# Optimization experiments

Hardware: AMD Instinct MI355X
Metric: run time of the kernel (lower is better)

## Reference

```python
import jax, jax.numpy as jnp
import numpy as np

EMBED_DIM = 1024
NUM_HEADS = 16
HEAD_DIM = EMBED_DIM // NUM_HEADS
B, S = 2, 2048


def setup_inputs() -> dict:
    key = jax.random.key(0)
    ks = jax.random.split(key, 9)
    d = EMBED_DIM
    scale = 1.0 / np.sqrt(d)
    inp = {
        "x": jax.random.normal(ks[0], (B, S, d), dtype=jnp.float32),
        "mask": jnp.ones((B, S), dtype=jnp.int32),
        "Wq": jax.random.normal(ks[1], (d, d), dtype=jnp.float32) * scale,
        "bq": jnp.zeros((d,), dtype=jnp.float32),
        "Wk": jax.random.normal(ks[2], (d, d), dtype=jnp.float32) * scale,
        "bk": jnp.zeros((d,), dtype=jnp.float32),
        "Wv": jax.random.normal(ks[3], (d, d), dtype=jnp.float32) * scale,
        "bv": jnp.zeros((d,), dtype=jnp.float32),
        "Wo": jax.random.normal(ks[4], (d, d), dtype=jnp.float32) * scale,
        "bo": jnp.zeros((d,), dtype=jnp.float32),
    }
    return inp


def reference(x, mask, Wq, bq, Wk, bk, Wv, bv, Wo, bo):
    b, s, _ = x.shape
    # projections; torch Linear computes x @ W.T + b
    q = (x @ Wq.T + bq).reshape(b, s, NUM_HEADS, HEAD_DIM).transpose(0, 2, 1, 3)
    k = (x @ Wk.T + bk).reshape(b, s, NUM_HEADS, HEAD_DIM).transpose(0, 2, 1, 3)
    v = (x @ Wv.T + bv).reshape(b, s, NUM_HEADS, HEAD_DIM).transpose(0, 2, 1, 3)
    scores = jnp.einsum("bhqd,bhkd->bhqk", q, k) / np.sqrt(HEAD_DIM)  # (B,H,S,S)
    m = (mask == 0)[:, None, None, :]  # broadcast over heads and query pos
    scores = jnp.where(m, jnp.float32(-1e9), scores)
    attn = jax.nn.softmax(scores, axis=-1)
    out = jnp.einsum("bhqk,bhkd->bhqd", attn, v)
    out = out.transpose(0, 2, 1, 3).reshape(b, s, EMBED_DIM)
    return out @ Wo.T + bo
```

## Files before the change

kernel.cpp:

```cpp
#include <hip/hip_runtime.h>

#define EMBED 1024
#define NHEAD 16
#define HDIM  64
#define BB    2
#define SS    2048

typedef __bf16 bf16x8 __attribute__((ext_vector_type(8)));
typedef float  f32x4  __attribute__((ext_vector_type(4)));
typedef _Float16 f16x4 __attribute__((ext_vector_type(4)));
typedef __fp16 hf16x2 __attribute__((ext_vector_type(2)));

#if defined(__has_builtin)
#if __has_builtin(__builtin_amdgcn_exp2f)
#define EXP2(x) __builtin_amdgcn_exp2f(x)
#else
#define EXP2(x) exp2f(x)
#endif
#else
#define EXP2(x) exp2f(x)
#endif

__device__ __forceinline__ unsigned short f2bf(float f) {
  union { float f; unsigned u; } v; v.f = f;
  unsigned r = v.u + 0x7fffu + ((v.u >> 16) & 1u);
  return (unsigned short)(r >> 16);
}

__device__ __forceinline__ float bf2f(unsigned short u) {
  union { unsigned u; float f; } v; v.u = ((unsigned)u) << 16;
  return v.f;
}

__device__ __forceinline__ unsigned short f2h(float f) {
  union { _Float16 h; unsigned short u; } t;
  t.h = (_Float16)f;
  return t.u;
}

__device__ __forceinline__ void g2l16(const unsigned short* g, unsigned short* l) {
  __builtin_amdgcn_global_load_lds(
      (const __attribute__((address_space(1))) unsigned int*)g,
      (__attribute__((address_space(3))) unsigned int*)l, 16, 0, 0);
}

__global__ __launch_bounds__(256)
void cvt5_kernel(const float* __restrict__ x,  const float* __restrict__ Wq,
                 const float* __restrict__ Wk, const float* __restrict__ Wv,
                 const float* __restrict__ Wo, const int* __restrict__ mask,
                 unsigned short* __restrict__ xb,  unsigned short* __restrict__ Wqb,
                 unsigned short* __restrict__ Wkb, unsigned short* __restrict__ Wvb,
                 unsigned short* __restrict__ Wob, float* __restrict__ mbias) {
  const int i = blockIdx.x * 256 + threadIdx.x;
  if (i < (1 << 21)) {
    const float* src;
    unsigned short* dst;
    int j;
    if (i < (1 << 20)) {
      src = x; dst = xb; j = i;
    } else {
      const int t = i - (1 << 20);
      const int r = t >> 18;
      j = t & ((1 << 18) - 1);
      src = (r == 0) ? Wq : (r == 1) ? Wk : (r == 2) ? Wv : Wo;
      dst = (r == 0) ? Wqb : (r == 1) ? Wkb : (r == 2) ? Wvb : Wob;
    }
    const float4 f = ((const float4*)src)[j];
    ushort4 u;
    u.x = f2bf(f.x); u.y = f2bf(f.y); u.z = f2bf(f.z); u.w = f2bf(f.w);
    ((ushort4*)dst)[j] = u;
  } else {
    const int j = i - (1 << 21);
    const int4 m = ((const int4*)mask)[j];
    float4 o;
    o.x = m.x ? 0.f : -1e30f; o.y = m.y ? 0.f : -1e30f;
    o.z = m.z ? 0.f : -1e30f; o.w = m.w ? 0.f : -1e30f;
    ((float4*)mbias)[j] = o;
  }
}

template <typename EpiFn>
__device__ __forceinline__
void gemm_core(const unsigned short* __restrict__ A,
               const unsigned short* __restrict__ Bm,
               int m0, int n0, EpiFn epi) {
  __shared__ unsigned short sA[128 * 64];
  __shared__ unsigned short sB[128 * 64];
  const int tid = threadIdx.x;
  const int l  = tid & 63;
  const int w  = tid >> 6;
  const int lm = l & 15;
  const int qd = l >> 4;
  const int wm = w & 1;
  const int wn = w >> 1;

  f32x4 acc[4][4];
#pragma unroll
  for (int i = 0; i < 4; ++i)
#pragma unroll
    for (int j = 0; j < 4; ++j) acc[i][j] = (f32x4){0.f, 0.f, 0.f, 0.f};

  for (int k0 = 0; k0 < EMBED; k0 += 64) {
#pragma unroll
    for (int i = 0; i < 4; ++i) {
      const int t = i * 256 + tid;
      const int r = t >> 3;
      const int c = (t & 7) ^ (r & 7);
      g2l16(A + (m0 + r) * EMBED + k0 + c * 8, &sA[(i * 256 + (w << 6)) * 8]);
      g2l16(Bm + (n0 + r) * EMBED + k0 + c * 8, &sB[(i * 256 + (w << 6)) * 8]);
    }
    __syncthreads();
#pragma unroll
    for (int kk = 0; kk < 2; ++kk) {
      bf16x8 af[4], bfr[4];
#pragma unroll
      for (int mi = 0; mi < 4; ++mi) {
        const int R = wm * 64 + mi * 16 + lm;
        const int ch = R * 8 + (((kk << 2) + qd) ^ (R & 7));
        af[mi] = *(const bf16x8*)&sA[ch * 8];
      }
#pragma unroll
      for (int ni = 0; ni < 4; ++ni) {
        const int R = wn * 64 + ni * 16 + lm;
        const int ch = R * 8 + (((kk << 2) + qd) ^ (R & 7));
        bfr[ni] = *(const bf16x8*)&sB[ch * 8];
      }
#pragma unroll
      for (int mi = 0; mi < 4; ++mi)
#pragma unroll
        for (int ni = 0; ni < 4; ++ni)
          acc[mi][ni] = __builtin_amdgcn_mfma_f32_16x16x32_bf16(
              af[mi], bfr[ni], acc[mi][ni], 0, 0, 0);
    }
    __syncthreads();
  }

#pragma unroll
  for (int mi = 0; mi < 4; ++mi)
#pragma unroll
    for (int ni = 0; ni < 4; ++ni) {
      const int mb = m0 + wm * 64 + mi * 16 + qd * 4;
      const int n  = n0 + wn * 64 + ni * 16 + lm;
      epi(acc[mi][ni], mb, n);
    }
}

__device__ __forceinline__ void decode_tile(int flat, int& a0, int& b0) {
  const int sub = flat & 15;
  const int g = flat >> 4;
  a0 = ((g >> 2) * 2 + (sub >> 3));
  b0 = ((g & 3) * 8 + (sub & 7));
}

__global__ __launch_bounds__(256)
void gemm_qkv(const unsigned short* __restrict__ xb,
              const unsigned short* __restrict__ Wqb,
              const unsigned short* __restrict__ Wkb,
              const unsigned short* __restrict__ Wvb,
              const float* __restrict__ bq, const float* __restrict__ bk,
              const float* __restrict__ bv,
              unsigned short* __restrict__ Qb, unsigned short* __restrict__ Kb,
              unsigned short* __restrict__ VTb) {
  const int z = blockIdx.y;
  int a0, b0;
  decode_tile(blockIdx.x, a0, b0);
  if (z < 2) {
    const unsigned short* A = z ? Wkb : Wqb;
    const float* bias = z ? bk : bq;
    unsigned short* O = z ? Kb : Qb;
    const float scale = z ? 1.0f : 0.125f * 1.4426950408889634f;
    gemm_core(A, xb, a0 * 128, b0 * 128, [&](const f32x4& v, int mb, int n) {
      const float4 bvv = *(const float4*)&bias[mb];
      const int h = mb >> 6, d0 = mb & 63;
      const int b = n >> 11, s = n & 2047;
      ushort4 u;
      u.x = f2bf((v.x + bvv.x) * scale); u.y = f2bf((v.y + bvv.y) * scale);
      u.z = f2bf((v.z + bvv.z) * scale); u.w = f2bf((v.w + bvv.w) * scale);
      *(ushort4*)&O[(((b * NHEAD + h) * SS) + s) * HDIM + d0] = u;
    });
  } else {
    gemm_core(xb, Wvb, b0 * 128, a0 * 128, [&](const f32x4& v, int mb, int n) {
      const float bvv = bv[n];
      const int b = mb >> 11, s = mb & 2047;
      const int h = n >> 6, d = n & 63;
      ushort4 u;
      u.x = f2h(v.x + bvv); u.y = f2h(v.y + bvv);
      u.z = f2h(v.z + bvv); u.w = f2h(v.w + bvv);
      *(ushort4*)&VTb[(((b * NHEAD + h) * HDIM) + d) * SS + s] = u;
    });
  }
}

__global__ __launch_bounds__(256)
void gemm_out(const unsigned short* __restrict__ Wob,
              const unsigned short* __restrict__ Ob,
              const float* __restrict__ bo, float* __restrict__ out) {
  int a0, b0;
  decode_tile(blockIdx.x, a0, b0);
  gemm_core(Wob, Ob, a0 * 128, b0 * 128, [&](const f32x4& v, int mb, int n) {
    const float4 bvv = *(const float4*)&bo[mb];
    float4 o;
    o.x = v.x + bvv.x; o.y = v.y + bvv.y; o.z = v.z + bvv.z; o.w = v.w + bvv.w;
    *(float4*)&out[n * EMBED + mb] = o;
  });
}

__global__ __launch_bounds__(256)
void attn_kernel(const unsigned short* __restrict__ Q,
                 const unsigned short* __restrict__ K,
                 const unsigned short* __restrict__ VT,
                 const float* __restrict__ mbias,
                 unsigned short* __restrict__ Opart,
                 float* __restrict__ Lpart) {
  __shared__ unsigned short sK[64 * 64];
  __shared__ unsigned short sV[64 * 64];
  const int tid = threadIdx.x;
  const int l = tid & 63, w = tid >> 6;
  const int lm = l & 15, qd = l >> 4;
  const int b = blockIdx.z & 1, sp = blockIdx.z >> 1, h = blockIdx.y;
  const int q0 = blockIdx.x * 128 + w * 32;
  const unsigned short* Qh = Q + ((b * NHEAD + h) * SS) * HDIM;
  const unsigned short* Kh = K + ((b * NHEAD + h) * SS) * HDIM;
  const unsigned short* Vh = VT + ((b * NHEAD + h) * HDIM) * SS;
  const float* mb = mbias + b * SS;
  unsigned short* Op = Opart + sp * (BB * SS * EMBED);
  float* Lp = Lpart + sp * (BB * NHEAD * SS);

  bf16x8 qf[2][2];
#pragma unroll
  for (int g = 0; g < 2; ++g) {
    qf[g][0] = *(const bf16x8*)&Qh[(q0 + g * 16 + lm) * HDIM + qd * 8];
    qf[g][1] = *(const bf16x8*)&Qh[(q0 + g * 16 + lm) * HDIM + 32 + qd * 8];
  }

  f32x4 Od[2][4];
#pragma unroll
  for (int g = 0; g < 2; ++g)
#pragma unroll
    for (int i = 0; i < 4; ++i) Od[g][i] = (f32x4){0.f, 0.f, 0.f, 0.f};
  float lsum[2] = {0.f, 0.f};

  const int kend = sp * (SS / 2) + (SS / 2);
  for (int kb = sp * (SS / 2); kb < kend; kb += 64) {
#pragma unroll
    for (int i = 0; i < 2; ++i) {
      const int t = i * 256 + tid;
      const int r = t >> 3;
      const int c = (t & 7) ^ (r & 7);
      g2l16(Kh + (kb + r) * HDIM + c * 8, &sK[(i * 256 + (w << 6)) * 8]);
      g2l16(Vh + r * SS + kb + c * 8, &sV[(i * 256 + (w << 6)) * 8]);
    }
    __syncthreads();

    f16x4 pf[2][4];
#pragma unroll
    for (int j = 0; j < 4; ++j) {
      const int R = j * 16 + lm;
      const bf16x8 k0 = *(const bf16x8*)&sK[(R * 8 + (qd ^ (lm & 7))) * 8];
      const bf16x8 k1 = *(const bf16x8*)&sK[(R * 8 + ((4 + qd) ^ (lm & 7))) * 8];
      const float4 bj = *(const float4*)&mb[kb + j * 16 + qd * 4];
      const f32x4 binit = (f32x4){bj.x, bj.y, bj.z, bj.w};
#pragma unroll
      for (int g = 0; g < 2; ++g) {
        f32x4 t0 = binit;
        t0 = __builtin_amdgcn_mfma_f32_16x16x32_bf16(k0, qf[g][0], t0, 0, 0, 0);
        t0 = __builtin_amdgcn_mfma_f32_16x16x32_bf16(k1, qf[g][1], t0, 0, 0, 0);
        const float p0 = EXP2(t0[0]);
        const float p1 = EXP2(t0[1]);
        const float p2 = EXP2(t0[2]);
        const float p3 = EXP2(t0[3]);
        lsum[g] += (p0 + p1) + (p2 + p3);
        union { hf16x2 v[2]; f16x4 f; } pk;
        pk.v[0] = __builtin_amdgcn_cvt_pkrtz(p0, p1);
        pk.v[1] = __builtin_amdgcn_cvt_pkrtz(p2, p3);
        pf[g][j] = pk.f;
      }
    }

#pragma unroll
    for (int dt = 0; dt < 4; ++dt) {
      const int row = dt * 16 + lm;
#pragma unroll
      for (int j = 0; j < 4; ++j) {
        const int ch = (j * 2 + (qd >> 1)) ^ (lm & 7);
        const f16x4 vf = *(const f16x4*)&sV[row * 64 + ch * 8 + (qd & 1) * 4];
#pragma unroll
        for (int g = 0; g < 2; ++g)
          Od[g][dt] = __builtin_amdgcn_mfma_f32_16x16x16f16(vf, pf[g][j],
                                                            Od[g][dt], 0, 0, 0);
      }
    }
    __syncthreads();
  }

#pragma unroll
  for (int g = 0; g < 2; ++g) {
    float ls = lsum[g];
    ls += __shfl_xor(ls, 16);
    ls += __shfl_xor(ls, 32);
    if (qd == 0) Lp[(b * NHEAD + h) * SS + q0 + g * 16 + lm] = ls;
#pragma unroll
    for (int dt = 0; dt < 4; ++dt) {
      ushort4 u;
      u.x = f2bf(Od[g][dt][0]); u.y = f2bf(Od[g][dt][1]);
      u.z = f2bf(Od[g][dt][2]); u.w = f2bf(Od[g][dt][3]);
      *(ushort4*)&Op[(b * SS + q0 + g * 16 + lm) * EMBED + h * HDIM +
                     dt * 16 + qd * 4] = u;
    }
  }
}

__global__ __launch_bounds__(256)
void combine_kernel(const unsigned short* __restrict__ Opart,
                    const float* __restrict__ Lpart,
                    unsigned short* __restrict__ Ob) {
  const int i = blockIdx.x * 256 + threadIdx.x;
  const int base = i * 8;
  const int token = base >> 10;
  const int h = (base >> 6) & 15;
  const int b = token >> 11, q = token & 2047;
  const int lidx = (b * NHEAD + h) * SS + q;
  const float ls = Lpart[lidx] + Lpart[BB * NHEAD * SS + lidx];
  const float rinv = 1.f / ls;
  const ushort4* p0 = (const ushort4*)&Opart[base];
  const ushort4* p1 = (const ushort4*)&Opart[BB * SS * EMBED + base];
  ushort4 o[2];
#pragma unroll
  for (int k = 0; k < 2; ++k) {
    const ushort4 a = p0[k], c = p1[k];
    o[k].x = f2bf((bf2f(a.x) + bf2f(c.x)) * rinv);
    o[k].y = f2bf((bf2f(a.y) + bf2f(c.y)) * rinv);
    o[k].z = f2bf((bf2f(a.z) + bf2f(c.z)) * rinv);
    o[k].w = f2bf((bf2f(a.w) + bf2f(c.w)) * rinv);
  }
  *(ushort4*)&Ob[base] = o[0];
  *(ushort4*)&Ob[base + 4] = o[1];
}

extern "C" void kernel_launch(void* const* d_in, const int* in_sizes, int n_in,
                              void* d_out, int out_size, void* d_ws, size_t ws_size,
                              hipStream_t stream) {
  const float* x  = (const float*)d_in[0];
  const int* mask = (const int*)d_in[1];
  const float* Wq = (const float*)d_in[2];
  const float* bq = (const float*)d_in[3];
  const float* Wk = (const float*)d_in[4];
  const float* bk = (const float*)d_in[5];
  const float* Wv = (const float*)d_in[6];
  const float* bv = (const float*)d_in[7];
  const float* Wo = (const float*)d_in[8];
  const float* bo = (const float*)d_in[9];
  float* out = (float*)d_out;

  char* ws = (char*)d_ws;
  const size_t MB = 1024 * 1024;
  unsigned short* xb  = (unsigned short*)(ws);
  unsigned short* Ob  = (unsigned short*)(ws);
  unsigned short* Wqb = (unsigned short*)(ws + 8 * MB);
  unsigned short* Wkb = Wqb + 1024 * 1024;
  unsigned short* Wvb = Wkb + 1024 * 1024;
  unsigned short* Wob = Wvb + 1024 * 1024;
  unsigned short* Qb  = (unsigned short*)(ws + 16 * MB);
  unsigned short* Kb  = (unsigned short*)(ws + 24 * MB);
  unsigned short* VTb = (unsigned short*)(ws + 32 * MB);
  unsigned short* Opart = (unsigned short*)(ws + 40 * MB);
  float* mbb   = (float*)(ws + 56 * MB);
  float* Lpart = (float*)(ws + 56 * MB + 64 * 1024);

  cvt5_kernel<<<8196, 256, 0, stream>>>(x, Wq, Wk, Wv, Wo, mask,
                                        xb, Wqb, Wkb, Wvb, Wob, mbb);
  gemm_qkv<<<dim3(256, 3), 256, 0, stream>>>(xb, Wqb, Wkb, Wvb, bq, bk, bv,
                                             Qb, Kb, VTb);
  attn_kernel<<<dim3(16, 16, 4), 256, 0, stream>>>(Qb, Kb, VTb, mbb,
                                                   Opart, Lpart);
  combine_kernel<<<2048, 256, 0, stream>>>(Opart, Lpart, Ob);
  gemm_out<<<256, 256, 0, stream>>>(Wob, Ob, bo, out);
}
```

Baseline: 218.5 us.

## Split attention keys three ways and permute V layout for wider LDS reads

The attention key range is split into three uneven chunks (704/704/640) instead of two, which raises the grid from 1024 to 1536 blocks so the GPU's compute units are better filled. The V-transpose store now permutes sequence positions inside each 32-key group, so the PV stage can load eight fp16 values per LDS read instead of four. The combine kernel sums three partials and writes the result in place into the first partial buffer, and the workspace is re-laid out so the third partial reuses the dead xb region. In exchange, the combine stage has more partial-output traffic to read, and the V permutation must match the P fragment ordering exactly.

```diff
diff --git a/kernel.cpp b/kernel.cpp
--- a/kernel.cpp
+++ b/kernel.cpp
@@ -9,6 +9,7 @@
 typedef __bf16 bf16x8 __attribute__((ext_vector_type(8)));
 typedef float  f32x4  __attribute__((ext_vector_type(4)));
 typedef _Float16 f16x4 __attribute__((ext_vector_type(4)));
+typedef _Float16 f16x8 __attribute__((ext_vector_type(8)));
 typedef __fp16 hf16x2 __attribute__((ext_vector_type(2)));
 
 #if defined(__has_builtin)
@@ -183,10 +184,11 @@
       const float bvv = bv[n];
       const int b = mb >> 11, s = mb & 2047;
       const int h = n >> 6, d = n & 63;
+      const int col = (s & ~31) + ((s >> 2) & 3) * 8 + ((s >> 4) & 1) * 4;
       ushort4 u;
       u.x = f2h(v.x + bvv); u.y = f2h(v.y + bvv);
       u.z = f2h(v.z + bvv); u.w = f2h(v.w + bvv);
-      *(ushort4*)&VTb[(((b * NHEAD + h) * HDIM) + d) * SS + s] = u;
+      *(ushort4*)&VTb[(((b * NHEAD + h) * HDIM) + d) * SS + col] = u;
     });
   }
 }
@@ -210,7 +212,9 @@
                  const unsigned short* __restrict__ K,
                  const unsigned short* __restrict__ VT,
                  const float* __restrict__ mbias,
-                 unsigned short* __restrict__ Opart,
+                 unsigned short* __restrict__ Op0,
+                 unsigned short* __restrict__ Op1,
+                 unsigned short* __restrict__ Op2,
                  float* __restrict__ Lpart) {
   __shared__ unsigned short sK[64 * 64];
   __shared__ unsigned short sV[64 * 64];
@@ -223,7 +227,7 @@
   const unsigned short* Kh = K + ((b * NHEAD + h) * SS) * HDIM;
   const unsigned short* Vh = VT + ((b * NHEAD + h) * HDIM) * SS;
   const float* mb = mbias + b * SS;
-  unsigned short* Op = Opart + sp * (BB * SS * EMBED);
+  unsigned short* Op = (sp == 0) ? Op0 : (sp == 1) ? Op1 : Op2;
   float* Lp = Lpart + sp * (BB * NHEAD * SS);
 
   bf16x8 qf[2][2];
@@ -240,8 +244,9 @@
     for (int i = 0; i < 4; ++i) Od[g][i] = (f32x4){0.f, 0.f, 0.f, 0.f};
   float lsum[2] = {0.f, 0.f};
 
-  const int kend = sp * (SS / 2) + (SS / 2);
-  for (int kb = sp * (SS / 2); kb < kend; kb += 64) {
+  const int k0 = (sp == 0) ? 0 : (sp == 1) ? 704 : 1408;
+  const int k1 = (sp == 0) ? 704 : (sp == 1) ? 1408 : 2048;
+  for (int kb = k0; kb < k1; kb += 64) {
 #pragma unroll
     for (int i = 0; i < 2; ++i) {
       const int t = i * 256 + tid;
@@ -256,15 +261,15 @@
 #pragma unroll
     for (int j = 0; j < 4; ++j) {
       const int R = j * 16 + lm;
-      const bf16x8 k0 = *(const bf16x8*)&sK[(R * 8 + (qd ^ (lm & 7))) * 8];
-      const bf16x8 k1 = *(const bf16x8*)&sK[(R * 8 + ((4 + qd) ^ (lm & 7))) * 8];
+      const bf16x8 k0f = *(const bf16x8*)&sK[(R * 8 + (qd ^ (lm & 7))) * 8];
+      const bf16x8 k1f = *(const bf16x8*)&sK[(R * 8 + ((4 + qd) ^ (lm & 7))) * 8];
       const float4 bj = *(const float4*)&mb[kb + j * 16 + qd * 4];
       const f32x4 binit = (f32x4){bj.x, bj.y, bj.z, bj.w};
 #pragma unroll
       for (int g = 0; g < 2; ++g) {
         f32x4 t0 = binit;
-        t0 = __builtin_amdgcn_mfma_f32_16x16x32_bf16(k0, qf[g][0], t0, 0, 0, 0);
-        t0 = __builtin_amdgcn_mfma_f32_16x16x32_bf16(k1, qf[g][1], t0, 0, 0, 0);
+        t0 = __builtin_amdgcn_mfma_f32_16x16x32_bf16(k0f, qf[g][0], t0, 0, 0, 0);
+        t0 = __builtin_amdgcn_mfma_f32_16x16x32_bf16(k1f, qf[g][1], t0, 0, 0, 0);
         const float p0 = EXP2(t0[0]);
         const float p1 = EXP2(t0[1]);
         const float p2 = EXP2(t0[2]);
@@ -281,13 +286,18 @@
     for (int dt = 0; dt < 4; ++dt) {
       const int row = dt * 16 + lm;
 #pragma unroll
-      for (int j = 0; j < 4; ++j) {
-        const int ch = (j * 2 + (qd >> 1)) ^ (lm & 7);
-        const f16x4 vf = *(const f16x4*)&sV[row * 64 + ch * 8 + (qd & 1) * 4];
-#pragma unroll
-        for (int g = 0; g < 2; ++g)
-          Od[g][dt] = __builtin_amdgcn_mfma_f32_16x16x16f16(vf, pf[g][j],
+      for (int p = 0; p < 2; ++p) {
+        const int ch = (p * 4 + qd) ^ (lm & 7);
+        const f16x8 v8 = *(const f16x8*)&sV[row * 64 + ch * 8];
+        const f16x4 vlo = __builtin_shufflevector(v8, v8, 0, 1, 2, 3);
+        const f16x4 vhi = __builtin_shufflevector(v8, v8, 4, 5, 6, 7);
+#pragma unroll
+        for (int g = 0; g < 2; ++g) {
+          Od[g][dt] = __builtin_amdgcn_mfma_f32_16x16x16f16(vlo, pf[g][2 * p],
                                                             Od[g][dt], 0, 0, 0);
+          Od[g][dt] = __builtin_amdgcn_mfma_f32_16x16x16f16(vhi, pf[g][2 * p + 1],
+                                                            Od[g][dt], 0, 0, 0);
+        }
       }
     }
     __syncthreads();
@@ -311,30 +321,31 @@
 }
 
 __global__ __launch_bounds__(256)
-void combine_kernel(const unsigned short* __restrict__ Opart,
-                    const float* __restrict__ Lpart,
-                    unsigned short* __restrict__ Ob) {
+void combine_kernel(unsigned short* __restrict__ Op0,
+                    const unsigned short* __restrict__ Op1,
+                    const unsigned short* __restrict__ Op2,
+                    const float* __restrict__ Lpart) {
   const int i = blockIdx.x * 256 + threadIdx.x;
   const int base = i * 8;
   const int token = base >> 10;
   const int h = (base >> 6) & 15;
   const int b = token >> 11, q = token & 2047;
   const int lidx = (b * NHEAD + h) * SS + q;
-  const float ls = Lpart[lidx] + Lpart[BB * NHEAD * SS + lidx];
+  const int LN = BB * NHEAD * SS;
+  const float ls = Lpart[lidx] + Lpart[LN + lidx] + Lpart[2 * LN + lidx];
   const float rinv = 1.f / ls;
-  const ushort4* p0 = (const ushort4*)&Opart[base];
-  const ushort4* p1 = (const ushort4*)&Opart[BB * SS * EMBED + base];
-  ushort4 o[2];
 #pragma unroll
   for (int k = 0; k < 2; ++k) {
-    const ushort4 a = p0[k], c = p1[k];
-    o[k].x = f2bf((bf2f(a.x) + bf2f(c.x)) * rinv);
-    o[k].y = f2bf((bf2f(a.y) + bf2f(c.y)) * rinv);
-    o[k].z = f2bf((bf2f(a.z) + bf2f(c.z)) * rinv);
-    o[k].w = f2bf((bf2f(a.w) + bf2f(c.w)) * rinv);
-  }
-  *(ushort4*)&Ob[base] = o[0];
-  *(ushort4*)&Ob[base + 4] = o[1];
+    const ushort4 a = *(const ushort4*)&Op0[base + k * 4];
+    const ushort4 c = *(const ushort4*)&Op1[base + k * 4];
+    const ushort4 d = *(const ushort4*)&Op2[base + k * 4];
+    ushort4 o;
+    o.x = f2bf((bf2f(a.x) + bf2f(c.x) + bf2f(d.x)) * rinv);
+    o.y = f2bf((bf2f(a.y) + bf2f(c.y) + bf2f(d.y)) * rinv);
+    o.z = f2bf((bf2f(a.z) + bf2f(c.z) + bf2f(d.z)) * rinv);
+    o.w = f2bf((bf2f(a.w) + bf2f(c.w) + bf2f(d.w)) * rinv);
+    *(ushort4*)&Op0[base + k * 4] = o;
+  }
 }
 
 extern "C" void kernel_launch(void* const* d_in, const int* in_sizes, int n_in,
@@ -355,24 +366,25 @@
   char* ws = (char*)d_ws;
   const size_t MB = 1024 * 1024;
   unsigned short* xb  = (unsigned short*)(ws);
-  unsigned short* Ob  = (unsigned short*)(ws);
   unsigned short* Wqb = (unsigned short*)(ws + 8 * MB);
-  unsigned short* Wkb = Wqb + 1024 * 1024;
-  unsigned short* Wvb = Wkb + 1024 * 1024;
-  unsigned short* Wob = Wvb + 1024 * 1024;
+  unsigned short* Wkb = (unsigned short*)(ws + 10 * MB);
+  unsigned short* Wvb = (unsigned short*)(ws + 12 * MB);
+  unsigned short* Wob = (unsigned short*)(ws + 14 * MB);
   unsigned short* Qb  = (unsigned short*)(ws + 16 * MB);
   unsigned short* Kb  = (unsigned short*)(ws + 24 * MB);
   unsigned short* VTb = (unsigned short*)(ws + 32 * MB);
-  unsigned short* Opart = (unsigned short*)(ws + 40 * MB);
-  float* mbb   = (float*)(ws + 56 * MB);
-  float* Lpart = (float*)(ws + 56 * MB + 64 * 1024);
+  float* mbb   = (float*)(ws + 40 * MB);
+  float* Lpart = (float*)(ws + 40 * MB + 64 * 1024);
+  unsigned short* Op0 = (unsigned short*)(ws + 41 * MB);
+  unsigned short* Op1 = (unsigned short*)(ws + 49 * MB);
+  unsigned short* Op2 = (unsigned short*)(ws);
 
   cvt5_kernel<<<8196, 256, 0, stream>>>(x, Wq, Wk, Wv, Wo, mask,
                                         xb, Wqb, Wkb, Wvb, Wob, mbb);
   gemm_qkv<<<dim3(256, 3), 256, 0, stream>>>(xb, Wqb, Wkb, Wvb, bq, bk, bv,
                                              Qb, Kb, VTb);
-  attn_kernel<<<dim3(16, 16, 4), 256, 0, stream>>>(Qb, Kb, VTb, mbb,
-                                                   Opart, Lpart);
-  combine_kernel<<<2048, 256, 0, stream>>>(Opart, Lpart, Ob);
-  gemm_out<<<256, 256, 0, stream>>>(Wob, Ob, bo, out);
-}
+  attn_kernel<<<dim3(16, 16, 6), 256, 0, stream>>>(Qb, Kb, VTb, mbb,
+                                                   Op0, Op1, Op2, Lpart);
+  combine_kernel<<<2048, 256, 0, stream>>>(Op0, Op1, Op2, Lpart);
+  gemm_out<<<256, 256, 0, stream>>>(Wob, Op0, bo, out);
+}
```

Measured after the change: 223.7 us. 2.4% more time.
